# Kernel tuning notes

Measured on AMD Instinct MI355X. Metric: run time of the kernel, lower is better.

Reference implementation:

```python
import jax, jax.numpy as jnp
import numpy as np

B, N_HOP, N_MEM, DIM = 1024, 2, 32, 64


def setup_inputs() -> dict:
    key = jax.random.key(0)
    ks = jax.random.split(key, 8)
    # Xavier-ish scales for linear weights
    def xav(k, shape):
        fan_in = shape[-1]
        return jax.random.normal(k, shape, dtype=jnp.float32) * (1.0 / np.sqrt(fan_in))
    return {
        "hs": jax.random.normal(ks[0], (B, N_HOP, N_MEM, DIM), dtype=jnp.float32),
        "Rs": jax.random.normal(ks[1], (B, N_HOP, N_MEM, DIM, DIM), dtype=jnp.float32) * (1.0 / np.sqrt(DIM)),
        "ts": jax.random.normal(ks[2], (B, N_HOP, N_MEM, DIM), dtype=jnp.float32),
        "vs": jax.random.normal(ks[3], (B, DIM), dtype=jnp.float32),
        "W1_w": xav(ks[4], (DIM, 4 * DIM)),
        "W1_b": jnp.zeros((DIM,), dtype=jnp.float32),
        "W2_w": xav(ks[5], (1, DIM)),
        "W2_b": jnp.zeros((1,), dtype=jnp.float32),
        "Wmem_w": xav(ks[6], (N_HOP, DIM, 3 * DIM)),
        "Wmem_b": jnp.zeros((N_HOP, DIM), dtype=jnp.float32),
        "z_w": xav(ks[7], (DIM, 2 * DIM)),
        "z_b": jnp.zeros((DIM,), dtype=jnp.float32),
    }


def reference(hs, Rs, ts, vs, W1_w, W1_b, W2_w, W2_b, Wmem_w, Wmem_b, z_w, z_b):
    """Faithful RippleNetPlus.forward (eval mode: dropout is identity)."""
    M = vs  # prev_mem
    o = vs  # v passed into EpisodicMemory each hop
    n_hop = hs.shape[1]
    for hop in range(n_hop):
        R = Rs[:, hop]   # [B, M, D, D]
        h = hs[:, hop]   # [B, M, D]
        t = ts[:, hop]   # [B, M, D]
        # batched GEMV replacing the B*n_memory Python-loop matmuls
        Rh = jnp.einsum('bmde,bme->bmd', R, h)  # [B, M, D]
        v = o[:, None, :]       # [B, 1, D]
        pm = M[:, None, :]      # [B, 1, D]
        z = jnp.concatenate(
            [Rh * v, Rh * pm, jnp.abs(Rh - v), jnp.abs(Rh - pm)], axis=-1)  # [B, M, 4D]
        hcode = jnp.tanh(jnp.einsum('bmf,df->bmd', z, W1_w) + W1_b)
        Z = (jnp.einsum('bmd,od->bmo', hcode, W2_w) + W2_b)[..., 0]  # [B, M]
        g = jax.nn.softmax(Z, axis=1)[..., None]                     # [B, M, 1]
        o_new = jnp.sum(t * g, axis=1)                               # [B, D]
        concat = jnp.concatenate([M, o_new, o], axis=1)              # [B, 3D]
        M = jax.nn.relu(concat @ Wmem_w[hop].T + Wmem_b[hop])
        o = o_new
    # AnswerModule
    u = jnp.concatenate([M, vs], axis=1) @ z_w.T + z_b  # [B, D]
    return jnp.sum(vs * u, axis=1)  # [B]
```

## Files before the change

kernel.cpp:

```cpp
#include <hip/hip_runtime.h>
#include <math.h>

#define NHOP 2
#define MEM 32
#define DIM 64

__global__ __launch_bounds__(256) void ripple_fwd(
    const float* __restrict__ hs,
    const float* __restrict__ Rs,
    const float* __restrict__ ts,
    const float* __restrict__ vs,
    const float* __restrict__ W1_w,
    const float* __restrict__ W1_b,
    const float* __restrict__ W2_w,
    const float* __restrict__ W2_b,
    const float* __restrict__ Wmem_w,
    const float* __restrict__ Wmem_b,
    const float* __restrict__ z_w,
    const float* __restrict__ z_b,
    float* __restrict__ out)
{
    __shared__ float W1T[256][64];
    __shared__ float Rh_sm[MEM][DIM + 1];
    __shared__ float M_sm[DIM], o_sm[DIM], onew_sm[DIM], vs_sm[DIM];
    __shared__ float Z_sm[MEM], g_sm[MEM];

    const int b   = blockIdx.x;
    const int tid = threadIdx.x;

    #pragma unroll 8
    for (int k = 0; k < 64; ++k)
        W1T[tid][k] = W1_w[k * 256 + tid];

    if (tid < DIM) {
        const float v = vs[b * DIM + tid];
        M_sm[tid] = v; o_sm[tid] = v; vs_sm[tid] = v;
    }
    __syncthreads();

    for (int hop = 0; hop < NHOP; ++hop) {
        const float* __restrict__ hbase = hs + (size_t)(b * NHOP + hop) * MEM * DIM;
        const float* __restrict__ Rbase = Rs + (size_t)(b * NHOP + hop) * MEM * DIM * DIM;
        const float* __restrict__ tbase = ts + (size_t)(b * NHOP + hop) * MEM * DIM;

        {
            const int l  = tid & 63;
            const int wv = tid >> 6;
            const int e0 = l & 3;
            const int dq = l >> 2;
            #pragma unroll 2
            for (int k = 0; k < 8; ++k) {
                const int m = k * 4 + wv;
                const float* __restrict__ Rm = Rbase + (size_t)m * DIM * DIM;
                const float* __restrict__ hm = hbase + m * DIM;
                const float4 hv0 = *reinterpret_cast<const float4*>(hm + 4 * e0);
                const float4 hv1 = *reinterpret_cast<const float4*>(hm + 4 * e0 + 16);
                const float4 hv2 = *reinterpret_cast<const float4*>(hm + 4 * e0 + 32);
                const float4 hv3 = *reinterpret_cast<const float4*>(hm + 4 * e0 + 48);
                #pragma unroll
                for (int dblk = 0; dblk < 4; ++dblk) {
                    const int d = dblk * 16 + dq;
                    const float* __restrict__ row = Rm + d * DIM + 4 * e0;
                    const float4 r0 = *reinterpret_cast<const float4*>(row);
                    const float4 r1 = *reinterpret_cast<const float4*>(row + 16);
                    const float4 r2 = *reinterpret_cast<const float4*>(row + 32);
                    const float4 r3 = *reinterpret_cast<const float4*>(row + 48);
                    float p = r0.x*hv0.x + r0.y*hv0.y + r0.z*hv0.z + r0.w*hv0.w;
                    p = fmaf(r1.x, hv1.x, fmaf(r1.y, hv1.y, fmaf(r1.z, hv1.z, fmaf(r1.w, hv1.w, p))));
                    p = fmaf(r2.x, hv2.x, fmaf(r2.y, hv2.y, fmaf(r2.z, hv2.z, fmaf(r2.w, hv2.w, p))));
                    p = fmaf(r3.x, hv3.x, fmaf(r3.y, hv3.y, fmaf(r3.z, hv3.z, fmaf(r3.w, hv3.w, p))));
                    p += __shfl_xor(p, 1);
                    p += __shfl_xor(p, 2);
                    if (e0 == 0) Rh_sm[m][d] = p;
                }
            }
        }
        __syncthreads();

        {
            const int d4 = tid & 15;
            const int mg = tid >> 4;
            float acc0[4] = {0.f, 0.f, 0.f, 0.f};
            float acc1[4] = {0.f, 0.f, 0.f, 0.f};
            #pragma unroll 4
            for (int e = 0; e < 64; ++e) {
                const float4 w0 = *reinterpret_cast<const float4*>(&W1T[e      ][d4 * 4]);
                const float4 w1 = *reinterpret_cast<const float4*>(&W1T[64  + e][d4 * 4]);
                const float4 w2 = *reinterpret_cast<const float4*>(&W1T[128 + e][d4 * 4]);
                const float4 w3 = *reinterpret_cast<const float4*>(&W1T[192 + e][d4 * 4]);
                const float oe  = o_sm[e];
                const float Me  = M_sm[e];
                const float rh0 = Rh_sm[mg][e];
                const float rh1 = Rh_sm[mg + 16][e];
                {
                    const float z0 = rh0 * oe, z1 = rh0 * Me;
                    const float z2 = fabsf(rh0 - oe), z3 = fabsf(rh0 - Me);
                    acc0[0] = fmaf(z0, w0.x, fmaf(z1, w1.x, fmaf(z2, w2.x, fmaf(z3, w3.x, acc0[0]))));
                    acc0[1] = fmaf(z0, w0.y, fmaf(z1, w1.y, fmaf(z2, w2.y, fmaf(z3, w3.y, acc0[1]))));
                    acc0[2] = fmaf(z0, w0.z, fmaf(z1, w1.z, fmaf(z2, w2.z, fmaf(z3, w3.z, acc0[2]))));
                    acc0[3] = fmaf(z0, w0.w, fmaf(z1, w1.w, fmaf(z2, w2.w, fmaf(z3, w3.w, acc0[3]))));
                }
                {
                    const float z0 = rh1 * oe, z1 = rh1 * Me;
                    const float z2 = fabsf(rh1 - oe), z3 = fabsf(rh1 - Me);
                    acc1[0] = fmaf(z0, w0.x, fmaf(z1, w1.x, fmaf(z2, w2.x, fmaf(z3, w3.x, acc1[0]))));
                    acc1[1] = fmaf(z0, w0.y, fmaf(z1, w1.y, fmaf(z2, w2.y, fmaf(z3, w3.y, acc1[1]))));
                    acc1[2] = fmaf(z0, w0.z, fmaf(z1, w1.z, fmaf(z2, w2.z, fmaf(z3, w3.z, acc1[2]))));
                    acc1[3] = fmaf(z0, w0.w, fmaf(z1, w1.w, fmaf(z2, w2.w, fmaf(z3, w3.w, acc1[3]))));
                }
            }
            float p0 = 0.f, p1 = 0.f;
            #pragma unroll
            for (int k2 = 0; k2 < 4; ++k2) {
                const int dd = d4 * 4 + k2;
                const float w2v = W2_w[dd];
                p0 += tanhf(acc0[k2] + W1_b[dd]) * w2v;
                p1 += tanhf(acc1[k2] + W1_b[dd]) * w2v;
            }
            #pragma unroll
            for (int s = 1; s < 16; s <<= 1) {
                p0 += __shfl_xor(p0, s, 64);
                p1 += __shfl_xor(p1, s, 64);
            }
            if (d4 == 0) {
                Z_sm[mg]      = p0 + W2_b[0];
                Z_sm[mg + 16] = p1 + W2_b[0];
            }
        }
        __syncthreads();

        if (tid < MEM) {
            float mx = Z_sm[0];
            #pragma unroll
            for (int m = 1; m < MEM; ++m) mx = fmaxf(mx, Z_sm[m]);
            float s = 0.f;
            #pragma unroll
            for (int m = 0; m < MEM; ++m) s += __expf(Z_sm[m] - mx);
            g_sm[tid] = __expf(Z_sm[tid] - mx) / s;
        }
        __syncthreads();

        if (tid < DIM) {
            float acc = 0.f;
            #pragma unroll 8
            for (int m = 0; m < MEM; ++m)
                acc += tbase[m * DIM + tid] * g_sm[m];
            onew_sm[tid] = acc;
        }
        __syncthreads();

        float Mn = 0.f;
        if (tid < DIM) {
            const float* __restrict__ Wm = Wmem_w + (size_t)(hop * DIM + tid) * 192;
            float acc = Wmem_b[hop * DIM + tid];
            #pragma unroll
            for (int k = 0; k < 16; ++k) {
                const float4 w = *reinterpret_cast<const float4*>(Wm + 4 * k);
                acc += w.x * M_sm[4*k] + w.y * M_sm[4*k+1] + w.z * M_sm[4*k+2] + w.w * M_sm[4*k+3];
            }
            #pragma unroll
            for (int k = 0; k < 16; ++k) {
                const float4 w = *reinterpret_cast<const float4*>(Wm + 64 + 4 * k);
                acc += w.x * onew_sm[4*k] + w.y * onew_sm[4*k+1] + w.z * onew_sm[4*k+2] + w.w * onew_sm[4*k+3];
            }
            #pragma unroll
            for (int k = 0; k < 16; ++k) {
                const float4 w = *reinterpret_cast<const float4*>(Wm + 128 + 4 * k);
                acc += w.x * o_sm[4*k] + w.y * o_sm[4*k+1] + w.z * o_sm[4*k+2] + w.w * o_sm[4*k+3];
            }
            Mn = fmaxf(acc, 0.f);
        }
        __syncthreads();
        if (tid < DIM) {
            M_sm[tid] = Mn;
            o_sm[tid] = onew_sm[tid];
        }
        __syncthreads();
    }

    if (tid < DIM) {
        const float* __restrict__ zr = z_w + (size_t)tid * 128;
        float u = z_b[tid];
        #pragma unroll
        for (int k = 0; k < 16; ++k) {
            const float4 w = *reinterpret_cast<const float4*>(zr + 4 * k);
            u += w.x * M_sm[4*k] + w.y * M_sm[4*k+1] + w.z * M_sm[4*k+2] + w.w * M_sm[4*k+3];
        }
        #pragma unroll
        for (int k = 0; k < 16; ++k) {
            const float4 w = *reinterpret_cast<const float4*>(zr + 64 + 4 * k);
            u += w.x * vs_sm[4*k] + w.y * vs_sm[4*k+1] + w.z * vs_sm[4*k+2] + w.w * vs_sm[4*k+3];
        }
        float r = vs_sm[tid] * u;
        #pragma unroll
        for (int s = 1; s < 64; s <<= 1) r += __shfl_xor(r, s, 64);
        if (tid == 0) out[b] = r;
    }
}

extern "C" void kernel_launch(void* const* d_in, const int* in_sizes, int n_in,
                              void* d_out, int out_size, void* d_ws, size_t ws_size,
                              hipStream_t stream)
{
    const float* hs     = (const float*)d_in[0];
    const float* Rs     = (const float*)d_in[1];
    const float* ts     = (const float*)d_in[2];
    const float* vs     = (const float*)d_in[3];
    const float* W1_w   = (const float*)d_in[4];
    const float* W1_b   = (const float*)d_in[5];
    const float* W2_w   = (const float*)d_in[6];
    const float* W2_b   = (const float*)d_in[7];
    const float* Wmem_w = (const float*)d_in[8];
    const float* Wmem_b = (const float*)d_in[9];
    const float* z_w    = (const float*)d_in[10];
    const float* z_b    = (const float*)d_in[11];
    float* out = (float*)d_out;

    const int B = out_size;
    ripple_fwd<<<B, 256, 0, stream>>>(hs, Rs, ts, vs, W1_w, W1_b, W2_w, W2_b,
                                      Wmem_w, Wmem_b, z_w, z_b, out);
}
```

Before: 217.7 us.

## Prefetch second-hop Rh into registers and fuse softmax with memory update

Both hops' R·h GEMVs are now computed up front. Hop-1 results are held in registers and written to shared memory after hop 0's scoring, so the two hops' large R loads are issued back to back instead of being separated by the dependent compute. The softmax, weighted sum and memory update are fused into a single wavefront, which drops several block barriers. The change also uses an exp-based tanh, transposes W1 into shared memory with vector loads, and sets a minimum of 2 blocks per CU in the launch bounds. The extra register array may raise register pressure, and the kernel stays dominated by streaming Rs from HBM.

```diff
diff --git a/kernel.cpp b/kernel.cpp
--- a/kernel.cpp
+++ b/kernel.cpp
@@ -5,7 +5,12 @@
 #define MEM 32
 #define DIM 64
 
-__global__ __launch_bounds__(256) void ripple_fwd(
+__device__ __forceinline__ float fast_tanh(float x) {
+    const float e = __expf(2.f * x);
+    return 1.f - 2.f / (e + 1.f);
+}
+
+__global__ __launch_bounds__(256, 2) void ripple_fwd(
     const float* __restrict__ hs,
     const float* __restrict__ Rs,
     const float* __restrict__ ts,
@@ -23,59 +28,100 @@
     __shared__ float W1T[256][64];
     __shared__ float Rh_sm[MEM][DIM + 1];
     __shared__ float M_sm[DIM], o_sm[DIM], onew_sm[DIM], vs_sm[DIM];
-    __shared__ float Z_sm[MEM], g_sm[MEM];
+    __shared__ float Z_sm[MEM];
 
     const int b   = blockIdx.x;
     const int tid = threadIdx.x;
-
-    #pragma unroll 8
-    for (int k = 0; k < 64; ++k)
-        W1T[tid][k] = W1_w[k * 256 + tid];
-
+    const int l   = tid & 63;
+    const int wv  = tid >> 6;
+
+    {
+        const int d  = l;
+        const int fq = wv;
+        #pragma unroll
+        for (int j = 0; j < 16; ++j) {
+            const int f = fq * 64 + j * 4;
+            const float4 w = *reinterpret_cast<const float4*>(W1_w + d * 256 + f);
+            W1T[f + 0][d] = w.x;
+            W1T[f + 1][d] = w.y;
+            W1T[f + 2][d] = w.z;
+            W1T[f + 3][d] = w.w;
+        }
+    }
     if (tid < DIM) {
         const float v = vs[b * DIM + tid];
         M_sm[tid] = v; o_sm[tid] = v; vs_sm[tid] = v;
     }
+
+    const int e0 = l & 3;
+    const int dq = l >> 2;
+
+    {
+        const float* __restrict__ Rbase = Rs + (size_t)(b * NHOP) * MEM * DIM * DIM;
+        const float* __restrict__ hbase = hs + (size_t)(b * NHOP) * MEM * DIM;
+        #pragma unroll 2
+        for (int k = 0; k < 8; ++k) {
+            const int m = k * 4 + wv;
+            const float* __restrict__ Rm = Rbase + (size_t)m * DIM * DIM;
+            const float* __restrict__ hm = hbase + m * DIM;
+            const float4 hv0 = *reinterpret_cast<const float4*>(hm + 4 * e0);
+            const float4 hv1 = *reinterpret_cast<const float4*>(hm + 4 * e0 + 16);
+            const float4 hv2 = *reinterpret_cast<const float4*>(hm + 4 * e0 + 32);
+            const float4 hv3 = *reinterpret_cast<const float4*>(hm + 4 * e0 + 48);
+            #pragma unroll
+            for (int dblk = 0; dblk < 4; ++dblk) {
+                const int d = dblk * 16 + dq;
+                const float* __restrict__ row = Rm + d * DIM + 4 * e0;
+                const float4 r0 = *reinterpret_cast<const float4*>(row);
+                const float4 r1 = *reinterpret_cast<const float4*>(row + 16);
+                const float4 r2 = *reinterpret_cast<const float4*>(row + 32);
+                const float4 r3 = *reinterpret_cast<const float4*>(row + 48);
+                float p = r0.x*hv0.x + r0.y*hv0.y + r0.z*hv0.z + r0.w*hv0.w;
+                p = fmaf(r1.x, hv1.x, fmaf(r1.y, hv1.y, fmaf(r1.z, hv1.z, fmaf(r1.w, hv1.w, p))));
+                p = fmaf(r2.x, hv2.x, fmaf(r2.y, hv2.y, fmaf(r2.z, hv2.z, fmaf(r2.w, hv2.w, p))));
+                p = fmaf(r3.x, hv3.x, fmaf(r3.y, hv3.y, fmaf(r3.z, hv3.z, fmaf(r3.w, hv3.w, p))));
+                p += __shfl_xor(p, 1);
+                p += __shfl_xor(p, 2);
+                if (e0 == 0) Rh_sm[m][d] = p;
+            }
+        }
+    }
     __syncthreads();
 
+    float a1[8][4];
+    {
+        const float* __restrict__ Rbase = Rs + ((size_t)(b * NHOP) + 1) * MEM * DIM * DIM;
+        const float* __restrict__ hbase = hs + ((size_t)(b * NHOP) + 1) * MEM * DIM;
+        #pragma unroll
+        for (int k = 0; k < 8; ++k) {
+            const int m = k * 4 + wv;
+            const float* __restrict__ Rm = Rbase + (size_t)m * DIM * DIM;
+            const float* __restrict__ hm = hbase + m * DIM;
+            const float4 hv0 = *reinterpret_cast<const float4*>(hm + 4 * e0);
+            const float4 hv1 = *reinterpret_cast<const float4*>(hm + 4 * e0 + 16);
+            const float4 hv2 = *reinterpret_cast<const float4*>(hm + 4 * e0 + 32);
+            const float4 hv3 = *reinterpret_cast<const float4*>(hm + 4 * e0 + 48);
+            #pragma unroll
+            for (int dblk = 0; dblk < 4; ++dblk) {
+                const int d = dblk * 16 + dq;
+                const float* __restrict__ row = Rm + d * DIM + 4 * e0;
+                const float4 r0 = *reinterpret_cast<const float4*>(row);
+                const float4 r1 = *reinterpret_cast<const float4*>(row + 16);
+                const float4 r2 = *reinterpret_cast<const float4*>(row + 32);
+                const float4 r3 = *reinterpret_cast<const float4*>(row + 48);
+                float p = r0.x*hv0.x + r0.y*hv0.y + r0.z*hv0.z + r0.w*hv0.w;
+                p = fmaf(r1.x, hv1.x, fmaf(r1.y, hv1.y, fmaf(r1.z, hv1.z, fmaf(r1.w, hv1.w, p))));
+                p = fmaf(r2.x, hv2.x, fmaf(r2.y, hv2.y, fmaf(r2.z, hv2.z, fmaf(r2.w, hv2.w, p))));
+                p = fmaf(r3.x, hv3.x, fmaf(r3.y, hv3.y, fmaf(r3.z, hv3.z, fmaf(r3.w, hv3.w, p))));
+                p += __shfl_xor(p, 1);
+                p += __shfl_xor(p, 2);
+                a1[k][dblk] = p;
+            }
+        }
+    }
+
     for (int hop = 0; hop < NHOP; ++hop) {
-        const float* __restrict__ hbase = hs + (size_t)(b * NHOP + hop) * MEM * DIM;
-        const float* __restrict__ Rbase = Rs + (size_t)(b * NHOP + hop) * MEM * DIM * DIM;
         const float* __restrict__ tbase = ts + (size_t)(b * NHOP + hop) * MEM * DIM;
-
-        {
-            const int l  = tid & 63;
-            const int wv = tid >> 6;
-            const int e0 = l & 3;
-            const int dq = l >> 2;
-            #pragma unroll 2
-            for (int k = 0; k < 8; ++k) {
-                const int m = k * 4 + wv;
-                const float* __restrict__ Rm = Rbase + (size_t)m * DIM * DIM;
-                const float* __restrict__ hm = hbase + m * DIM;
-                const float4 hv0 = *reinterpret_cast<const float4*>(hm + 4 * e0);
-                const float4 hv1 = *reinterpret_cast<const float4*>(hm + 4 * e0 + 16);
-                const float4 hv2 = *reinterpret_cast<const float4*>(hm + 4 * e0 + 32);
-                const float4 hv3 = *reinterpret_cast<const float4*>(hm + 4 * e0 + 48);
-                #pragma unroll
-                for (int dblk = 0; dblk < 4; ++dblk) {
-                    const int d = dblk * 16 + dq;
-                    const float* __restrict__ row = Rm + d * DIM + 4 * e0;
-                    const float4 r0 = *reinterpret_cast<const float4*>(row);
-                    const float4 r1 = *reinterpret_cast<const float4*>(row + 16);
-                    const float4 r2 = *reinterpret_cast<const float4*>(row + 32);
-                    const float4 r3 = *reinterpret_cast<const float4*>(row + 48);
-                    float p = r0.x*hv0.x + r0.y*hv0.y + r0.z*hv0.z + r0.w*hv0.w;
-                    p = fmaf(r1.x, hv1.x, fmaf(r1.y, hv1.y, fmaf(r1.z, hv1.z, fmaf(r1.w, hv1.w, p))));
-                    p = fmaf(r2.x, hv2.x, fmaf(r2.y, hv2.y, fmaf(r2.z, hv2.z, fmaf(r2.w, hv2.w, p))));
-                    p = fmaf(r3.x, hv3.x, fmaf(r3.y, hv3.y, fmaf(r3.z, hv3.z, fmaf(r3.w, hv3.w, p))));
-                    p += __shfl_xor(p, 1);
-                    p += __shfl_xor(p, 2);
-                    if (e0 == 0) Rh_sm[m][d] = p;
-                }
-            }
-        }
-        __syncthreads();
 
         {
             const int d4 = tid & 15;
@@ -114,8 +160,8 @@
             for (int k2 = 0; k2 < 4; ++k2) {
                 const int dd = d4 * 4 + k2;
                 const float w2v = W2_w[dd];
-                p0 += tanhf(acc0[k2] + W1_b[dd]) * w2v;
-                p1 += tanhf(acc1[k2] + W1_b[dd]) * w2v;
+                p0 += fast_tanh(acc0[k2] + W1_b[dd]) * w2v;
+                p1 += fast_tanh(acc1[k2] + W1_b[dd]) * w2v;
             }
             #pragma unroll
             for (int s = 1; s < 16; s <<= 1) {
@@ -129,53 +175,51 @@
         }
         __syncthreads();
 
-        if (tid < MEM) {
+        if (hop == 0) {
+            #pragma unroll
+            for (int k = 0; k < 8; ++k) {
+                const int m = k * 4 + wv;
+                #pragma unroll
+                for (int dblk = 0; dblk < 4; ++dblk)
+                    if (e0 == 0) Rh_sm[m][dblk * 16 + dq] = a1[k][dblk];
+            }
+        }
+
+        if (tid < DIM) {
             float mx = Z_sm[0];
             #pragma unroll
             for (int m = 1; m < MEM; ++m) mx = fmaxf(mx, Z_sm[m]);
             float s = 0.f;
             #pragma unroll
             for (int m = 0; m < MEM; ++m) s += __expf(Z_sm[m] - mx);
-            g_sm[tid] = __expf(Z_sm[tid] - mx) / s;
-        }
-        __syncthreads();
-
-        if (tid < DIM) {
             float acc = 0.f;
-            #pragma unroll 8
+            #pragma unroll
             for (int m = 0; m < MEM; ++m)
-                acc += tbase[m * DIM + tid] * g_sm[m];
-            onew_sm[tid] = acc;
-        }
-        __syncthreads();
-
-        float Mn = 0.f;
-        if (tid < DIM) {
+                acc = fmaf(tbase[m * DIM + tid], __expf(Z_sm[m] - mx), acc);
+            const float onew = acc / s;
+            onew_sm[tid] = onew;
+
             const float* __restrict__ Wm = Wmem_w + (size_t)(hop * DIM + tid) * 192;
-            float acc = Wmem_b[hop * DIM + tid];
+            float acc2 = Wmem_b[hop * DIM + tid];
             #pragma unroll
             for (int k = 0; k < 16; ++k) {
                 const float4 w = *reinterpret_cast<const float4*>(Wm + 4 * k);
-                acc += w.x * M_sm[4*k] + w.y * M_sm[4*k+1] + w.z * M_sm[4*k+2] + w.w * M_sm[4*k+3];
+                acc2 += w.x * M_sm[4*k] + w.y * M_sm[4*k+1] + w.z * M_sm[4*k+2] + w.w * M_sm[4*k+3];
             }
             #pragma unroll
             for (int k = 0; k < 16; ++k) {
                 const float4 w = *reinterpret_cast<const float4*>(Wm + 64 + 4 * k);
-                acc += w.x * onew_sm[4*k] + w.y * onew_sm[4*k+1] + w.z * onew_sm[4*k+2] + w.w * onew_sm[4*k+3];
+                acc2 += w.x * onew_sm[4*k] + w.y * onew_sm[4*k+1] + w.z * onew_sm[4*k+2] + w.w * onew_sm[4*k+3];
             }
             #pragma unroll
             for (int k = 0; k < 16; ++k) {
                 const float4 w = *reinterpret_cast<const float4*>(Wm + 128 + 4 * k);
-                acc += w.x * o_sm[4*k] + w.y * o_sm[4*k+1] + w.z * o_sm[4*k+2] + w.w * o_sm[4*k+3];
-            }
-            Mn = fmaxf(acc, 0.f);
-        }
-        __syncthreads();
-        if (tid < DIM) {
-            M_sm[tid] = Mn;
-            o_sm[tid] = onew_sm[tid];
-        }
-        __syncthreads();
+                acc2 += w.x * o_sm[4*k] + w.y * o_sm[4*k+1] + w.z * o_sm[4*k+2] + w.w * o_sm[4*k+3];
+            }
+            M_sm[tid] = fmaxf(acc2, 0.f);
+            o_sm[tid] = onew;
+        }
+        if (hop == 0) __syncthreads();
     }
 
     if (tid < DIM) {
```

Result: no change. 218.7 us (+0.4%).

## Use bf16 MFMA for the W1 projection and fuse softmax, weighted sum and memory update

Applied to the files above, without the earlier changes.

Replaces the scalar fp32 FMA loop for the 4D→D W1 projection with bf16 16x16x32 MFMA instructions. W1 is pre-packed in LDS in fragment order as bf16, which halves its LDS footprint, and launch bounds now ask for 3 blocks per CU. Softmax, the weighted sum over t and the Wmem update are merged into one single-wave section, which removes several block barriers; W2_b is dropped because softmax ignores a constant shift. The risk is bf16 rounding error in the attention logits, and the kernel stays dominated by streaming Rs from memory.

```diff
diff --git a/kernel.cpp b/kernel.cpp
--- a/kernel.cpp
+++ b/kernel.cpp
@@ -5,7 +5,21 @@
 #define MEM 32
 #define DIM 64
 
-__global__ __launch_bounds__(256) void ripple_fwd(
+typedef __attribute__((ext_vector_type(8))) short short8v;
+typedef __attribute__((ext_vector_type(4))) float f32x4;
+
+__device__ __forceinline__ float fast_tanh(float x) {
+    const float e = __expf(2.f * x);
+    return 1.f - 2.f / (e + 1.f);
+}
+
+__device__ __forceinline__ short bf16b(float x) {
+    union { float f; unsigned u; } c; c.f = x;
+    const unsigned r = c.u + 0x7fffu + ((c.u >> 16) & 1u);
+    return (short)(r >> 16);
+}
+
+__global__ __launch_bounds__(256, 3) void ripple_fwd(
     const float* __restrict__ hs,
     const float* __restrict__ Rs,
     const float* __restrict__ ts,
@@ -20,162 +34,167 @@
     const float* __restrict__ z_b,
     float* __restrict__ out)
 {
-    __shared__ float W1T[256][64];
-    __shared__ float Rh_sm[MEM][DIM + 1];
+    __shared__ uint4 W1B[32 * 64];
+    __shared__ float Rh_sm[MEM][68];
     __shared__ float M_sm[DIM], o_sm[DIM], onew_sm[DIM], vs_sm[DIM];
-    __shared__ float Z_sm[MEM], g_sm[MEM];
+    __shared__ float Zp[2][MEM];
+    __shared__ float cvec[128];
 
     const int b   = blockIdx.x;
     const int tid = threadIdx.x;
-
-    #pragma unroll 8
-    for (int k = 0; k < 64; ++k)
-        W1T[tid][k] = W1_w[k * 256 + tid];
-
+    const int l   = tid & 63;
+    const int wv  = tid >> 6;
+
+    #pragma unroll
+    for (int t = 0; t < 8; ++t) {
+        const int s    = t * 256 + tid;
+        const int frag = s >> 6, ll = s & 63;
+        const int kt = frag >> 2, nt = frag & 3;
+        const int n  = nt * 16 + (ll & 15);
+        const int f0 = kt * 32 + (ll >> 4) * 8;
+        const float4 wa = *reinterpret_cast<const float4*>(W1_w + n * 256 + f0);
+        const float4 wb = *reinterpret_cast<const float4*>(W1_w + n * 256 + f0 + 4);
+        short8v v;
+        v[0] = bf16b(wa.x); v[1] = bf16b(wa.y); v[2] = bf16b(wa.z); v[3] = bf16b(wa.w);
+        v[4] = bf16b(wb.x); v[5] = bf16b(wb.y); v[6] = bf16b(wb.z); v[7] = bf16b(wb.w);
+        *reinterpret_cast<short8v*>(&W1B[s]) = v;
+    }
     if (tid < DIM) {
+        cvec[tid]      = W1_b[tid];
+        cvec[64 + tid] = W2_w[tid];
         const float v = vs[b * DIM + tid];
         M_sm[tid] = v; o_sm[tid] = v; vs_sm[tid] = v;
     }
-    __syncthreads();
+
+    const int e0s = l & 3;
+    const int dq  = l >> 2;
 
     for (int hop = 0; hop < NHOP; ++hop) {
+        const float* __restrict__ Rbase = Rs + (size_t)(b * NHOP + hop) * MEM * DIM * DIM;
         const float* __restrict__ hbase = hs + (size_t)(b * NHOP + hop) * MEM * DIM;
-        const float* __restrict__ Rbase = Rs + (size_t)(b * NHOP + hop) * MEM * DIM * DIM;
         const float* __restrict__ tbase = ts + (size_t)(b * NHOP + hop) * MEM * DIM;
 
+        #pragma unroll 2
+        for (int k = 0; k < 8; ++k) {
+            const int m = k * 4 + wv;
+            const float* __restrict__ Rm = Rbase + (size_t)m * DIM * DIM;
+            const float* __restrict__ hm = hbase + m * DIM;
+            const float4 hv0 = *reinterpret_cast<const float4*>(hm + 4 * e0s);
+            const float4 hv1 = *reinterpret_cast<const float4*>(hm + 4 * e0s + 16);
+            const float4 hv2 = *reinterpret_cast<const float4*>(hm + 4 * e0s + 32);
+            const float4 hv3 = *reinterpret_cast<const float4*>(hm + 4 * e0s + 48);
+            #pragma unroll
+            for (int dblk = 0; dblk < 4; ++dblk) {
+                const int d = dblk * 16 + dq;
+                const float* __restrict__ row = Rm + d * DIM + 4 * e0s;
+                const float4 r0 = *reinterpret_cast<const float4*>(row);
+                const float4 r1 = *reinterpret_cast<const float4*>(row + 16);
+                const float4 r2 = *reinterpret_cast<const float4*>(row + 32);
+                const float4 r3 = *reinterpret_cast<const float4*>(row + 48);
+                float p = r0.x*hv0.x + r0.y*hv0.y + r0.z*hv0.z + r0.w*hv0.w;
+                p = fmaf(r1.x, hv1.x, fmaf(r1.y, hv1.y, fmaf(r1.z, hv1.z, fmaf(r1.w, hv1.w, p))));
+                p = fmaf(r2.x, hv2.x, fmaf(r2.y, hv2.y, fmaf(r2.z, hv2.z, fmaf(r2.w, hv2.w, p))));
+                p = fmaf(r3.x, hv3.x, fmaf(r3.y, hv3.y, fmaf(r3.z, hv3.z, fmaf(r3.w, hv3.w, p))));
+                p += __shfl_xor(p, 1);
+                p += __shfl_xor(p, 2);
+                if (e0s == 0) Rh_sm[m][d] = p;
+            }
+        }
+        __syncthreads();
+
         {
-            const int l  = tid & 63;
-            const int wv = tid >> 6;
-            const int e0 = l & 3;
-            const int dq = l >> 2;
-            #pragma unroll 2
-            for (int k = 0; k < 8; ++k) {
-                const int m = k * 4 + wv;
-                const float* __restrict__ Rm = Rbase + (size_t)m * DIM * DIM;
-                const float* __restrict__ hm = hbase + m * DIM;
-                const float4 hv0 = *reinterpret_cast<const float4*>(hm + 4 * e0);
-                const float4 hv1 = *reinterpret_cast<const float4*>(hm + 4 * e0 + 16);
-                const float4 hv2 = *reinterpret_cast<const float4*>(hm + 4 * e0 + 32);
-                const float4 hv3 = *reinterpret_cast<const float4*>(hm + 4 * e0 + 48);
+            const int g   = l >> 4;
+            const int col = l & 15;
+            const int mt  = wv & 1;
+            const int nh  = wv >> 1;
+            const int m   = mt * 16 + col;
+            f32x4 acc0 = {0.f, 0.f, 0.f, 0.f};
+            f32x4 acc1 = {0.f, 0.f, 0.f, 0.f};
+            #pragma unroll
+            for (int kt = 0; kt < 8; ++kt) {
+                const int part = kt >> 1;
+                const int e0 = (kt & 1) * 32 + g * 8;
+                const float4 r0 = *reinterpret_cast<const float4*>(&Rh_sm[m][e0]);
+                const float4 r1 = *reinterpret_cast<const float4*>(&Rh_sm[m][e0 + 4]);
+                const float* vsrc = (part & 1) ? M_sm : o_sm;
+                const float4 q0 = *reinterpret_cast<const float4*>(vsrc + e0);
+                const float4 q1 = *reinterpret_cast<const float4*>(vsrc + e0 + 4);
+                float zz[8];
+                if (part < 2) {
+                    zz[0] = r0.x*q0.x; zz[1] = r0.y*q0.y; zz[2] = r0.z*q0.z; zz[3] = r0.w*q0.w;
+                    zz[4] = r1.x*q1.x; zz[5] = r1.y*q1.y; zz[6] = r1.z*q1.z; zz[7] = r1.w*q1.w;
+                } else {
+                    zz[0] = fabsf(r0.x-q0.x); zz[1] = fabsf(r0.y-q0.y);
+                    zz[2] = fabsf(r0.z-q0.z); zz[3] = fabsf(r0.w-q0.w);
+                    zz[4] = fabsf(r1.x-q1.x); zz[5] = fabsf(r1.y-q1.y);
+                    zz[6] = fabsf(r1.z-q1.z); zz[7] = fabsf(r1.w-q1.w);
+                }
+                short8v a;
+                a[0] = bf16b(zz[0]); a[1] = bf16b(zz[1]); a[2] = bf16b(zz[2]); a[3] = bf16b(zz[3]);
+                a[4] = bf16b(zz[4]); a[5] = bf16b(zz[5]); a[6] = bf16b(zz[6]); a[7] = bf16b(zz[7]);
+                const short8v b0 = *reinterpret_cast<const short8v*>(&W1B[(kt * 4 + nh * 2 + 0) * 64 + l]);
+                const short8v b1 = *reinterpret_cast<const short8v*>(&W1B[(kt * 4 + nh * 2 + 1) * 64 + l]);
+                acc0 = __builtin_amdgcn_mfma_f32_16x16x32_bf16(a, b0, acc0, 0, 0, 0);
+                acc1 = __builtin_amdgcn_mfma_f32_16x16x32_bf16(a, b1, acc1, 0, 0, 0);
+            }
+            const int n0 = (nh * 2 + 0) * 16 + col;
+            const int n1 = (nh * 2 + 1) * 16 + col;
+            const float b1a = cvec[n0], b1b = cvec[n1];
+            const float w2a = cvec[64 + n0], w2b = cvec[64 + n1];
+            float pz[4];
+            #pragma unroll
+            for (int r = 0; r < 4; ++r)
+                pz[r] = fast_tanh(acc0[r] + b1a) * w2a + fast_tanh(acc1[r] + b1b) * w2b;
+            #pragma unroll
+            for (int s = 1; s < 16; s <<= 1) {
+                pz[0] += __shfl_xor(pz[0], s, 64);
+                pz[1] += __shfl_xor(pz[1], s, 64);
+                pz[2] += __shfl_xor(pz[2], s, 64);
+                pz[3] += __shfl_xor(pz[3], s, 64);
+            }
+            if (col == 0) {
                 #pragma unroll
-                for (int dblk = 0; dblk < 4; ++dblk) {
-                    const int d = dblk * 16 + dq;
-                    const float* __restrict__ row = Rm + d * DIM + 4 * e0;
-                    const float4 r0 = *reinterpret_cast<const float4*>(row);
-                    const float4 r1 = *reinterpret_cast<const float4*>(row + 16);
-                    const float4 r2 = *reinterpret_cast<const float4*>(row + 32);
-                    const float4 r3 = *reinterpret_cast<const float4*>(row + 48);
-                    float p = r0.x*hv0.x + r0.y*hv0.y + r0.z*hv0.z + r0.w*hv0.w;
-                    p = fmaf(r1.x, hv1.x, fmaf(r1.y, hv1.y, fmaf(r1.z, hv1.z, fmaf(r1.w, hv1.w, p))));
-                    p = fmaf(r2.x, hv2.x, fmaf(r2.y, hv2.y, fmaf(r2.z, hv2.z, fmaf(r2.w, hv2.w, p))));
-                    p = fmaf(r3.x, hv3.x, fmaf(r3.y, hv3.y, fmaf(r3.z, hv3.z, fmaf(r3.w, hv3.w, p))));
-                    p += __shfl_xor(p, 1);
-                    p += __shfl_xor(p, 2);
-                    if (e0 == 0) Rh_sm[m][d] = p;
-                }
+                for (int r = 0; r < 4; ++r)
+                    Zp[nh][mt * 16 + 4 * g + r] = pz[r];
             }
         }
         __syncthreads();
 
-        {
-            const int d4 = tid & 15;
-            const int mg = tid >> 4;
-            float acc0[4] = {0.f, 0.f, 0.f, 0.f};
-            float acc1[4] = {0.f, 0.f, 0.f, 0.f};
-            #pragma unroll 4
-            for (int e = 0; e < 64; ++e) {
-                const float4 w0 = *reinterpret_cast<const float4*>(&W1T[e      ][d4 * 4]);
-                const float4 w1 = *reinterpret_cast<const float4*>(&W1T[64  + e][d4 * 4]);
-                const float4 w2 = *reinterpret_cast<const float4*>(&W1T[128 + e][d4 * 4]);
-                const float4 w3 = *reinterpret_cast<const float4*>(&W1T[192 + e][d4 * 4]);
-                const float oe  = o_sm[e];
-                const float Me  = M_sm[e];
-                const float rh0 = Rh_sm[mg][e];
-                const float rh1 = Rh_sm[mg + 16][e];
-                {
-                    const float z0 = rh0 * oe, z1 = rh0 * Me;
-                    const float z2 = fabsf(rh0 - oe), z3 = fabsf(rh0 - Me);
-                    acc0[0] = fmaf(z0, w0.x, fmaf(z1, w1.x, fmaf(z2, w2.x, fmaf(z3, w3.x, acc0[0]))));
-                    acc0[1] = fmaf(z0, w0.y, fmaf(z1, w1.y, fmaf(z2, w2.y, fmaf(z3, w3.y, acc0[1]))));
-                    acc0[2] = fmaf(z0, w0.z, fmaf(z1, w1.z, fmaf(z2, w2.z, fmaf(z3, w3.z, acc0[2]))));
-                    acc0[3] = fmaf(z0, w0.w, fmaf(z1, w1.w, fmaf(z2, w2.w, fmaf(z3, w3.w, acc0[3]))));
-                }
-                {
-                    const float z0 = rh1 * oe, z1 = rh1 * Me;
-                    const float z2 = fabsf(rh1 - oe), z3 = fabsf(rh1 - Me);
-                    acc1[0] = fmaf(z0, w0.x, fmaf(z1, w1.x, fmaf(z2, w2.x, fmaf(z3, w3.x, acc1[0]))));
-                    acc1[1] = fmaf(z0, w0.y, fmaf(z1, w1.y, fmaf(z2, w2.y, fmaf(z3, w3.y, acc1[1]))));
-                    acc1[2] = fmaf(z0, w0.z, fmaf(z1, w1.z, fmaf(z2, w2.z, fmaf(z3, w3.z, acc1[2]))));
-                    acc1[3] = fmaf(z0, w0.w, fmaf(z1, w1.w, fmaf(z2, w2.w, fmaf(z3, w3.w, acc1[3]))));
-                }
-            }
-            float p0 = 0.f, p1 = 0.f;
-            #pragma unroll
-            for (int k2 = 0; k2 < 4; ++k2) {
-                const int dd = d4 * 4 + k2;
-                const float w2v = W2_w[dd];
-                p0 += tanhf(acc0[k2] + W1_b[dd]) * w2v;
-                p1 += tanhf(acc1[k2] + W1_b[dd]) * w2v;
-            }
-            #pragma unroll
-            for (int s = 1; s < 16; s <<= 1) {
-                p0 += __shfl_xor(p0, s, 64);
-                p1 += __shfl_xor(p1, s, 64);
-            }
-            if (d4 == 0) {
-                Z_sm[mg]      = p0 + W2_b[0];
-                Z_sm[mg + 16] = p1 + W2_b[0];
-            }
-        }
-        __syncthreads();
-
-        if (tid < MEM) {
-            float mx = Z_sm[0];
-            #pragma unroll
-            for (int m = 1; m < MEM; ++m) mx = fmaxf(mx, Z_sm[m]);
-            float s = 0.f;
-            #pragma unroll
-            for (int m = 0; m < MEM; ++m) s += __expf(Z_sm[m] - mx);
-            g_sm[tid] = __expf(Z_sm[tid] - mx) / s;
-        }
-        __syncthreads();
-
         if (tid < DIM) {
-            float acc = 0.f;
-            #pragma unroll 8
-            for (int m = 0; m < MEM; ++m)
-                acc += tbase[m * DIM + tid] * g_sm[m];
-            onew_sm[tid] = acc;
-        }
-        __syncthreads();
-
-        float Mn = 0.f;
-        if (tid < DIM) {
+            float mx = -1e30f;
+            #pragma unroll
+            for (int m = 0; m < MEM; ++m) mx = fmaxf(mx, Zp[0][m] + Zp[1][m]);
+            float s = 0.f, accn = 0.f;
+            #pragma unroll
+            for (int m = 0; m < MEM; ++m) {
+                const float e = __expf(Zp[0][m] + Zp[1][m] - mx);
+                s += e;
+                accn = fmaf(tbase[m * DIM + tid], e, accn);
+            }
+            const float onew = accn / s;
+            onew_sm[tid] = onew;
+
             const float* __restrict__ Wm = Wmem_w + (size_t)(hop * DIM + tid) * 192;
-            float acc = Wmem_b[hop * DIM + tid];
+            float acc2 = Wmem_b[hop * DIM + tid];
             #pragma unroll
             for (int k = 0; k < 16; ++k) {
                 const float4 w = *reinterpret_cast<const float4*>(Wm + 4 * k);
-                acc += w.x * M_sm[4*k] + w.y * M_sm[4*k+1] + w.z * M_sm[4*k+2] + w.w * M_sm[4*k+3];
+                acc2 += w.x * M_sm[4*k] + w.y * M_sm[4*k+1] + w.z * M_sm[4*k+2] + w.w * M_sm[4*k+3];
             }
             #pragma unroll
             for (int k = 0; k < 16; ++k) {
                 const float4 w = *reinterpret_cast<const float4*>(Wm + 64 + 4 * k);
-                acc += w.x * onew_sm[4*k] + w.y * onew_sm[4*k+1] + w.z * onew_sm[4*k+2] + w.w * onew_sm[4*k+3];
+                acc2 += w.x * onew_sm[4*k] + w.y * onew_sm[4*k+1] + w.z * onew_sm[4*k+2] + w.w * onew_sm[4*k+3];
             }
             #pragma unroll
             for (int k = 0; k < 16; ++k) {
                 const float4 w = *reinterpret_cast<const float4*>(Wm + 128 + 4 * k);
-                acc += w.x * o_sm[4*k] + w.y * o_sm[4*k+1] + w.z * o_sm[4*k+2] + w.w * o_sm[4*k+3];
-            }
-            Mn = fmaxf(acc, 0.f);
-        }
-        __syncthreads();
-        if (tid < DIM) {
-            M_sm[tid] = Mn;
-            o_sm[tid] = onew_sm[tid];
-        }
-        __syncthreads();
+                acc2 += w.x * o_sm[4*k] + w.y * o_sm[4*k+1] + w.z * o_sm[4*k+2] + w.w * o_sm[4*k+3];
+            }
+            M_sm[tid] = fmaxf(acc2, 0.f);
+            o_sm[tid] = onew;
+        }
+        if (hop == 0) __syncthreads();
     }
 
     if (tid < DIM) {
```

Result: no change. 215.5 us (-1.0%).
